# Kernel optimization log

Measured on AMD Instinct MI355X. Metric: run time of the kernel, lower is better.

Reference implementation:

```python
import jax, jax.numpy as jnp
import numpy as np

HID, NH, QLR, KVLR, QK, VH, RH = 7168, 128, 1536, 512, 128, 128, 64
EPS = 1.1920929e-07  # torch.finfo(float32).eps, RMSNorm eps=None default
ROPE_BASE = 10000.0


def _rmsnorm(x, w):
    return x * jax.lax.rsqrt(jnp.mean(x * x, axis=-1, keepdims=True) + EPS) * w


def _rope_tables(seq_len, dim):
    inv_freq = 1.0 / (ROPE_BASE ** (np.arange(0, dim, 2, dtype=np.float32) / dim))
    t = np.arange(seq_len, dtype=np.float32)
    freqs = np.outer(t, inv_freq)          # [S, dim/2]
    emb = np.concatenate([freqs, freqs], -1)  # [S, dim]
    return jnp.asarray(np.cos(emb)), jnp.asarray(np.sin(emb))


def _apply_rope(x, cos, sin):
    # x: [B, H, S, D]; rotate-half convention matching the torch module
    d = x.shape[-1]
    x1, x2 = x[..., : d // 2], x[..., d // 2 :]
    rotated = jnp.concatenate([-x2, x1], axis=-1)
    return x * cos + rotated * sin


def setup_inputs() -> dict:
    key = jax.random.key(0)
    ks = jax.random.split(key, 9)
    def w(k, out_dim, in_dim):
        return jax.random.normal(k, (out_dim, in_dim), jnp.float32) / np.sqrt(in_dim)
    return {
        "hidden_states": jax.random.normal(ks[0], (1, 1024, HID), jnp.float32),
        "w_q_down": w(ks[1], QLR, HID),
        "q_norm_w": jnp.ones((QLR,), jnp.float32),
        "w_q_up": w(ks[2], NH * (QK + RH), QLR),
        "w_kv_down": w(ks[3], KVLR + RH, HID),
        "kv_norm_w": jnp.ones((KVLR,), jnp.float32),
        "w_kv_up": w(ks[4], NH * (QK + VH), KVLR),
        "w_out": w(ks[5], HID, NH * VH),
    }


def reference(hidden_states, w_q_down, q_norm_w, w_q_up, w_kv_down, kv_norm_w, w_kv_up, w_out):
    B, S, _ = hidden_states.shape
    cos, sin = _rope_tables(S, RH)

    # Q path: down -> RMSNorm -> up, split into non-rope / rope parts
    c_q = jnp.einsum("bsh,qh->bsq", hidden_states, w_q_down)            # [B,S,QLR]
    q_cr = jnp.einsum("bsq,oq->bso", _rmsnorm(c_q, q_norm_w), w_q_up)   # [B,S,NH*(QK+RH)]
    q_cr = q_cr.reshape(B, S, NH, QK + RH).transpose(0, 2, 1, 3)        # [B,NH,S,QK+RH]
    q_c, q_r = q_cr[..., :QK], q_cr[..., QK:]

    # KV path: shared latent + MQA rope key
    ckv_kr = jnp.einsum("bsh,oh->bso", hidden_states, w_kv_down)        # [B,S,KVLR+RH]
    c_kv, k_r = ckv_kr[..., :KVLR], ckv_kr[..., KVLR:]
    k_r = k_r[:, None, :, :]                                            # [B,1,S,RH]
    kv = jnp.einsum("bsq,oq->bso", _rmsnorm(c_kv, kv_norm_w), w_kv_up)  # [B,S,NH*(QK+VH)]
    kv = kv.reshape(B, S, NH, QK + VH).transpose(0, 2, 1, 3)            # [B,NH,S,QK+VH]
    k_c, v = kv[..., :QK], kv[..., QK:]

    q_r = _apply_rope(q_r, cos, sin)
    k_r = _apply_rope(k_r, cos, sin)

    q = jnp.concatenate([q_c, q_r], axis=-1)                            # [B,NH,S,QK+RH]
    k = jnp.concatenate([k_c, jnp.broadcast_to(k_r, (B, NH, S, RH))], axis=-1)

    scale = 1.0 / np.sqrt(QK + RH)
    scores = jnp.einsum("bhqd,bhkd->bhqk", q, k) * scale
    attn = jax.nn.softmax(scores, axis=-1)
    o = jnp.einsum("bhqk,bhkd->bhqd", attn, v)                          # [B,NH,S,VH]
    o = o.transpose(0, 2, 1, 3).reshape(B, S, NH * VH)
    return jnp.einsum("bso,ho->bsh", o, w_out)
```

## Files before the change

kernel.cpp:

```cpp
#include <hip/hip_runtime.h>
#include <hip/hip_bf16.h>
#include <math.h>

#define HIDN 7168
#define NHEAD 128
#define QLRANK 1536
#define KVLRANK 512
#define QKD 128
#define VHD 128
#define RHD 64
#define SEQ 1024
#define RMS_EPS 1.1920929e-07f

typedef unsigned short u16;
typedef __attribute__((ext_vector_type(8))) short bf16x8;
typedef __attribute__((ext_vector_type(4))) float f32x4;
typedef __attribute__((ext_vector_type(8))) unsigned short u16x8;

__device__ __forceinline__ u16 f2bf(float f) {
    unsigned int u = __float_as_uint(f);
    unsigned int r = (u + 0x7FFFu + ((u >> 16) & 1u)) >> 16;
    return (u16)r;
}
__device__ __forceinline__ float bf2f(u16 v) {
    return __uint_as_float(((unsigned int)v) << 16);
}

__device__ __forceinline__ void gld_lds16(const u16* g, u16* l) {
    __builtin_amdgcn_global_load_lds(
        (const __attribute__((address_space(1))) unsigned int*)g,
        (__attribute__((address_space(3))) unsigned int*)l,
        16, 0, 0);
}

__global__ __launch_bounds__(256) void f32_to_bf16(const float* __restrict__ in,
                                                   u16* __restrict__ out, long n) {
    long i = ((long)blockIdx.x * blockDim.x + threadIdx.x) * 8;
    long stride = (long)gridDim.x * blockDim.x * 8;
    for (; i < n; i += stride) {
        float4 a = *(const float4*)(in + i);
        float4 b = *(const float4*)(in + i + 4);
        u16x8 o;
        o[0] = f2bf(a.x); o[1] = f2bf(a.y); o[2] = f2bf(a.z); o[3] = f2bf(a.w);
        o[4] = f2bf(b.x); o[5] = f2bf(b.y); o[6] = f2bf(b.z); o[7] = f2bf(b.w);
        *(u16x8*)(out + i) = o;
    }
}

template <int OUT_BF16>
__global__ __launch_bounds__(512) void gemm_bt(const u16* __restrict__ A,
                                               const u16* __restrict__ B,
                                               void* __restrict__ Cv,
                                               int M, int N, int Kslice, long ldk) {
    __shared__ u16 As[2 * 128 * 64];
    __shared__ u16 Bs[2 * 128 * 64];
    const int tid = threadIdx.x;
    const int lane = tid & 63;
    const int w = tid >> 6;
    const int wr = w >> 2, wc = w & 3;
    const int l15 = lane & 15, lg = lane >> 4;
    const int n0 = blockIdx.x * 128;
    const int m0 = blockIdx.y * 128;
    const long kbase = (long)blockIdx.z * Kslice;

    const u16* asrc[2];
    const u16* bsrc[2];
    int aoff[2];
#pragma unroll
    for (int i = 0; i < 2; ++i) {
        int r = (w * 2 + i) * 8 + (lane >> 3);
        int gc = (lane & 7) ^ (r & 7);
        asrc[i] = A + (long)(m0 + r) * ldk + kbase + gc * 8;
        int br = n0 + r; if (br >= N) br = N - 1;
        bsrc[i] = B + (long)br * ldk + kbase + gc * 8;
        aoff[i] = (w * 2 + i) * 512;
    }

    f32x4 acc[4][2];
    const f32x4 z = {0.f, 0.f, 0.f, 0.f};
#pragma unroll
    for (int i = 0; i < 4; ++i)
#pragma unroll
        for (int j = 0; j < 2; ++j) acc[i][j] = z;

    auto stage = [&](int bufi, int kofs) {
#pragma unroll
        for (int i = 0; i < 2; ++i) {
            gld_lds16(asrc[i] + kofs, As + bufi * 8192 + aoff[i]);
            gld_lds16(bsrc[i] + kofs, Bs + bufi * 8192 + aoff[i]);
        }
    };

    const int nsteps = Kslice >> 6;
    stage(0, 0);
    asm volatile("s_waitcnt vmcnt(0)" ::: "memory");
    __builtin_amdgcn_s_barrier();

    int cur = 0;
    for (int t = 0; t < nsteps; ++t) {
        if (t + 1 < nsteps) stage(cur ^ 1, (t + 1) * 64);
        const u16* Ab = As + cur * 8192;
        const u16* Bb = Bs + cur * 8192;
#pragma unroll
        for (int kk = 0; kk < 2; ++kk) {
            bf16x8 a[4], b[2];
#pragma unroll
            for (int i = 0; i < 4; ++i) {
                int row = wr * 64 + i * 16 + l15;
                a[i] = *(const bf16x8*)&Ab[row * 64 + ((kk * 4 + lg) ^ (row & 7)) * 8];
            }
#pragma unroll
            for (int j = 0; j < 2; ++j) {
                int row = wc * 32 + j * 16 + l15;
                b[j] = *(const bf16x8*)&Bb[row * 64 + ((kk * 4 + lg) ^ (row & 7)) * 8];
            }
#pragma unroll
            for (int i = 0; i < 4; ++i)
#pragma unroll
                for (int j = 0; j < 2; ++j)
                    acc[i][j] = __builtin_amdgcn_mfma_f32_16x16x32_bf16(a[i], b[j], acc[i][j], 0, 0, 0);
        }
        asm volatile("s_waitcnt vmcnt(0)" ::: "memory");
        __builtin_amdgcn_s_barrier();
        cur ^= 1;
    }

#pragma unroll
    for (int i = 0; i < 4; ++i)
#pragma unroll
        for (int j = 0; j < 2; ++j)
#pragma unroll
            for (int r = 0; r < 4; ++r) {
                int m = m0 + wr * 64 + i * 16 + lg * 4 + r;
                int n = n0 + wc * 32 + j * 16 + l15;
                if (n < N) {
                    if (OUT_BF16)
                        ((u16*)Cv)[(long)m * N + n] = f2bf(acc[i][j][r]);
                    else
                        ((float*)Cv)[(long)blockIdx.z * M * N + (long)m * N + n] = acc[i][j][r];
                }
            }
}

__global__ __launch_bounds__(256) void reduce_parts(const float* __restrict__ parts,
                                                    float* __restrict__ out,
                                                    int nparts, long mn) {
    long i = ((long)blockIdx.x * 256 + threadIdx.x) * 4;
    long stride = (long)gridDim.x * 256 * 4;
    for (; i < mn; i += stride) {
        float4 s = *(const float4*)(parts + i);
        for (int p = 1; p < nparts; ++p) {
            float4 v = *(const float4*)(parts + (long)p * mn + i);
            s.x += v.x; s.y += v.y; s.z += v.z; s.w += v.w;
        }
        *(float4*)(out + i) = s;
    }
}

__global__ __launch_bounds__(256) void rmsnorm_kernel(const float* __restrict__ x,
                                                      const float* __restrict__ w,
                                                      u16* __restrict__ y,
                                                      int stride, int norm_len) {
    const int row = blockIdx.x;
    const float* xr = x + (long)row * stride;
    float ss = 0.f;
    for (int i = threadIdx.x; i < norm_len; i += 256) {
        float v = xr[i];
        ss += v * v;
    }
#pragma unroll
    for (int off = 32; off > 0; off >>= 1) ss += __shfl_down(ss, off);
    __shared__ float partial[4];
    if ((threadIdx.x & 63) == 0) partial[threadIdx.x >> 6] = ss;
    __syncthreads();
    float tot = partial[0] + partial[1] + partial[2] + partial[3];
    float rs = 1.0f / sqrtf(tot / (float)norm_len + RMS_EPS);
    u16* yr = y + (long)row * norm_len;
    for (int i = threadIdx.x; i < norm_len; i += 256) yr[i] = f2bf(xr[i] * rs * w[i]);
}

__global__ void rope_tables(float* __restrict__ cos_t, float* __restrict__ sin_t) {
    int s = blockIdx.x;
    int i = threadIdx.x;
    float invf = powf(10000.0f, -((float)(2 * i) / 64.0f));
    float ang = (float)s * invf;
    cos_t[s * 32 + i] = cosf(ang);
    sin_t[s * 32 + i] = sinf(ang);
}

__global__ void rope_q(u16* __restrict__ q_cr, const float* __restrict__ cos_t,
                       const float* __restrict__ sin_t) {
    int s = blockIdx.x;
    int h = blockIdx.y * 2 + (threadIdx.x >> 5);
    int i = threadIdx.x & 31;
    u16* base = q_cr + (s * (NHEAD * 192) + h * 192 + QKD);
    float x1 = bf2f(base[i]);
    float x2 = bf2f(base[i + 32]);
    float c = cos_t[s * 32 + i], sn = sin_t[s * 32 + i];
    base[i]      = f2bf(x1 * c - x2 * sn);
    base[i + 32] = f2bf(x2 * c + x1 * sn);
}

__global__ void rope_k(const float* __restrict__ ckv_kr, const float* __restrict__ cos_t,
                       const float* __restrict__ sin_t, u16* __restrict__ kr) {
    int s = blockIdx.x;
    int i = threadIdx.x;
    if (i < 32) {
        const float* base = ckv_kr + (s * 576 + 512);
        float x1 = base[i], x2 = base[i + 32];
        float c = cos_t[s * 32 + i], sn = sin_t[s * 32 + i];
        kr[s * 64 + i]      = f2bf(x1 * c - x2 * sn);
        kr[s * 64 + i + 32] = f2bf(x2 * c + x1 * sn);
    }
}

__global__ __launch_bounds__(512) void mla_attn(const u16* __restrict__ q_cr,
                                                const u16* __restrict__ kv,
                                                const u16* __restrict__ kr,
                                                u16* __restrict__ o_g,
                                                const float* __restrict__ wsrc,
                                                u16* __restrict__ wdst,
                                                int do_conv) {
    __shared__ u16 ks[64][200];
    __shared__ u16 vts[128][72];
    __shared__ u16 p_lds[8][16][72];
    __shared__ u16 vtile[64][136];
    const int qb = blockIdx.x, h = blockIdx.y;
    const int s0q = qb * 128;
    const int tid = threadIdx.x, lane = tid & 63, w = tid >> 6;
    const int l15 = lane & 15, lg = lane >> 4;
    const float scale = 0.07216878364870323f;

    bf16x8 qreg[6];
    {
        const int qrow = s0q + w * 16 + l15;
#pragma unroll
        for (int kk = 0; kk < 6; ++kk)
            qreg[kk] = *(const bf16x8*)&q_cr[qrow * (NHEAD * 192) + h * 192 + kk * 32 + lg * 8];
    }

    const int krow0 = tid >> 4,           koff0 = (tid & 15) * 8;
    const int krow1 = (512 + tid) >> 4,   koff1 = ((512 + tid) & 15) * 8;
    const int rrow  = tid >> 3,           roff  = (tid & 7) * 8;
    const u16* kvp = kv + h * 256;
    const u16* kvv = kv + h * 256 + 128;

    u16x8 kreg0, kreg1, krreg, vreg0, vreg1;
    auto load_tile = [&](int s0k) {
        kreg0 = *(const u16x8*)&kvp[(long)(s0k + krow0) * 32768 + koff0];
        kreg1 = *(const u16x8*)&kvp[(long)(s0k + krow1) * 32768 + koff1];
        krreg = *(const u16x8*)&kr[(s0k + rrow) * 64 + roff];
        vreg0 = *(const u16x8*)&kvv[(long)(s0k + krow0) * 32768 + koff0];
        vreg1 = *(const u16x8*)&kvv[(long)(s0k + krow1) * 32768 + koff1];
    };

    const long cbase = ((long)(h * 8 + qb)) * 16 * 896;

    f32x4 o_acc[8];
    const f32x4 z = {0.f, 0.f, 0.f, 0.f};
#pragma unroll
    for (int d = 0; d < 8; ++d) o_acc[d] = z;
    float m_r[4], l_r[4];
#pragma unroll
    for (int r = 0; r < 4; ++r) { m_r[r] = -1e30f; l_r[r] = 0.f; }

    load_tile(0);

    for (int kt = 0; kt < 16; ++kt) {
        __syncthreads();
        *(u16x8*)&ks[krow0][koff0]      = kreg0;
        *(u16x8*)&ks[krow1][koff1]      = kreg1;
        *(u16x8*)&ks[rrow][128 + roff]  = krreg;
        *(u16x8*)&vtile[krow0][koff0]   = vreg0;
        *(u16x8*)&vtile[krow1][koff1]   = vreg1;
        __syncthreads();
        if (kt + 1 < 16) load_tile((kt + 1) * 64);

        if (do_conv) {
            long g0 = cbase + (long)kt * 896;
#pragma unroll
            for (int ci = 0; ci < 2; ++ci) {
                int gi = ci * 512 + tid;
                if (gi < 896) {
                    long g8 = (g0 + gi) * 8;
                    float4 a = *(const float4*)(wsrc + g8);
                    float4 b = *(const float4*)(wsrc + g8 + 4);
                    u16x8 o;
                    o[0] = f2bf(a.x); o[1] = f2bf(a.y); o[2] = f2bf(a.z); o[3] = f2bf(a.w);
                    o[4] = f2bf(b.x); o[5] = f2bf(b.y); o[6] = f2bf(b.z); o[7] = f2bf(b.w);
                    *(u16x8*)(wdst + g8) = o;
                }
            }
        }

        {
            const int dv = tid >> 2;
            const int sb = (tid & 3) << 4;
#pragma unroll
            for (int i = 0; i < 16; ++i)
                vts[dv][sb + i] = vtile[sb + i][dv];
        }

        f32x4 sf[4];
#pragma unroll
        for (int j = 0; j < 4; ++j) sf[j] = z;
        __builtin_amdgcn_s_setprio(1);
#pragma unroll
        for (int kk = 0; kk < 6; ++kk) {
            bf16x8 a = qreg[kk];
#pragma unroll
            for (int j = 0; j < 4; ++j) {
                bf16x8 b = *(const bf16x8*)&ks[j * 16 + l15][kk * 32 + lg * 8];
                sf[j] = __builtin_amdgcn_mfma_f32_16x16x32_bf16(a, b, sf[j], 0, 0, 0);
            }
        }
        __builtin_amdgcn_s_setprio(0);

        float p[4][4];
        float alpha[4];
#pragma unroll
        for (int r = 0; r < 4; ++r) {
            float mx = fmaxf(fmaxf(sf[0][r], sf[1][r]), fmaxf(sf[2][r], sf[3][r]));
#pragma unroll
            for (int off = 1; off < 16; off <<= 1) mx = fmaxf(mx, __shfl_xor(mx, off));
            mx *= scale;
            float mnew = fmaxf(m_r[r], mx);
            alpha[r] = __expf(m_r[r] - mnew);
            float rs = 0.f;
#pragma unroll
            for (int j = 0; j < 4; ++j) {
                float pv = __expf(sf[j][r] * scale - mnew);
                p[j][r] = pv;
                rs += pv;
            }
#pragma unroll
            for (int off = 1; off < 16; off <<= 1) rs += __shfl_xor(rs, off);
            l_r[r] = l_r[r] * alpha[r] + rs;
            m_r[r] = mnew;
        }
#pragma unroll
        for (int d = 0; d < 8; ++d)
#pragma unroll
            for (int r = 0; r < 4; ++r) o_acc[d][r] *= alpha[r];

#pragma unroll
        for (int j = 0; j < 4; ++j)
#pragma unroll
            for (int r = 0; r < 4; ++r)
                p_lds[w][lg * 4 + r][j * 16 + l15] = f2bf(p[j][r]);

        __syncthreads();

        __builtin_amdgcn_s_setprio(1);
#pragma unroll
        for (int kk2 = 0; kk2 < 2; ++kk2) {
            bf16x8 a = *(const bf16x8*)&p_lds[w][l15][kk2 * 32 + lg * 8];
#pragma unroll
            for (int d = 0; d < 8; ++d) {
                bf16x8 b = *(const bf16x8*)&vts[d * 16 + l15][kk2 * 32 + lg * 8];
                o_acc[d] = __builtin_amdgcn_mfma_f32_16x16x32_bf16(a, b, o_acc[d], 0, 0, 0);
            }
        }
        __builtin_amdgcn_s_setprio(0);
    }

#pragma unroll
    for (int d = 0; d < 8; ++d)
#pragma unroll
        for (int r = 0; r < 4; ++r) {
            int srow = s0q + w * 16 + lg * 4 + r;
            float v = o_acc[d][r] / l_r[r];
            o_g[srow * 16384 + h * 128 + d * 16 + l15] = f2bf(v);
        }
}

extern "C" void kernel_launch(void* const* d_in, const int* in_sizes, int n_in,
                              void* d_out, int out_size, void* d_ws, size_t ws_size,
                              hipStream_t stream) {
    const float* hs        = (const float*)d_in[0];
    const float* w_q_down  = (const float*)d_in[1];
    const float* q_norm_w  = (const float*)d_in[2];
    const float* w_q_up    = (const float*)d_in[3];
    const float* w_kv_down = (const float*)d_in[4];
    const float* kv_norm_w = (const float*)d_in[5];
    const float* w_kv_up   = (const float*)d_in[6];
    const float* w_out     = (const float*)d_in[7];
    float* out = (float*)d_out;
    char* ws = (char*)d_ws;

    const size_t SZ_KV   = (size_t)SEQ * 32768 * 2;
    const size_t SZ_QCR  = (size_t)SEQ * (NHEAD * 192) * 2;
    const size_t SZ_KR   = (size_t)SEQ * 64 * 2;
    const size_t SZ_OG   = (size_t)SEQ * 16384 * 2;
    const size_t SZ_TAB  = (size_t)SEQ * 32 * 4;
    const size_t SZ_WOUT = (size_t)HIDN * 16384 * 2;
    const size_t SZ_WB   = (size_t)24576 * 1536 * 2;
    const size_t SZ_PART = (size_t)4 * SEQ * QLRANK * 4;
    const size_t SZ_HS   = (size_t)SEQ * HIDN * 2;
    const size_t SZ_CQ   = (size_t)SEQ * QLRANK * 4;
    const size_t SZ_CQN  = (size_t)SEQ * QLRANK * 2;
    const size_t SZ_CKV  = (size_t)SEQ * 576 * 4;
    const size_t SZ_CKVN = (size_t)SEQ * KVLRANK * 2;

    size_t off = 0;
    u16* kvb     = (u16*)(ws + off); off += SZ_KV;
    u16* q_cr    = (u16*)(ws + off); off += SZ_QCR;
    u16* kr      = (u16*)(ws + off); off += SZ_KR;
    u16* o_g     = (u16*)(ws + off); off += SZ_OG;
    float* cos_t = (float*)(ws + off); off += SZ_TAB;
    float* sin_t = (float*)(ws + off); off += SZ_TAB;
    const size_t live_end = off;
    u16* wout_bf = (u16*)(ws + live_end);
    u16* W_BUF   = (u16*)(ws + live_end);
    float* parts = (float*)(ws + live_end + SZ_WB);
    size_t toff = live_end + SZ_WB + SZ_PART;
    u16* hs_bf    = (u16*)(ws + toff); toff += SZ_HS;
    float* c_q    = (float*)(ws + toff); toff += SZ_CQ;
    u16* cq_n     = (u16*)(ws + toff); toff += SZ_CQN;
    float* ckv_kr = (float*)(ws + toff); toff += SZ_CKV;
    u16* ckv_n    = (u16*)(ws + toff); toff += SZ_CKVN;
    const int fuse = (live_end + SZ_WOUT) <= ws_size;
    (void)in_sizes; (void)n_in; (void)out_size;

    rope_tables<<<dim3(SEQ), dim3(32), 0, stream>>>(cos_t, sin_t);
    f32_to_bf16<<<2048, 256, 0, stream>>>(hs, hs_bf, (long)SEQ * HIDN);

    f32_to_bf16<<<2048, 256, 0, stream>>>(w_q_down, W_BUF, (long)QLRANK * HIDN);
    gemm_bt<0><<<dim3(QLRANK / 128, SEQ / 128, 4), 512, 0, stream>>>(hs_bf, W_BUF, parts, SEQ, QLRANK, HIDN / 4, HIDN);
    reduce_parts<<<1024, 256, 0, stream>>>(parts, c_q, 4, (long)SEQ * QLRANK);
    rmsnorm_kernel<<<SEQ, 256, 0, stream>>>(c_q, q_norm_w, cq_n, QLRANK, QLRANK);

    f32_to_bf16<<<2048, 256, 0, stream>>>(w_q_up, W_BUF, (long)24576 * QLRANK);
    gemm_bt<1><<<dim3(24576 / 128, SEQ / 128), 512, 0, stream>>>(cq_n, W_BUF, q_cr, SEQ, 24576, QLRANK, QLRANK);

    f32_to_bf16<<<2048, 256, 0, stream>>>(w_kv_down, W_BUF, (long)576 * HIDN);
    gemm_bt<0><<<dim3(5, SEQ / 128, 8), 512, 0, stream>>>(hs_bf, W_BUF, parts, SEQ, 576, HIDN / 8, HIDN);
    reduce_parts<<<1024, 256, 0, stream>>>(parts, ckv_kr, 8, (long)SEQ * 576);
    rmsnorm_kernel<<<SEQ, 256, 0, stream>>>(ckv_kr, kv_norm_w, ckv_n, 576, KVLRANK);
    rope_k<<<SEQ, 64, 0, stream>>>(ckv_kr, cos_t, sin_t, kr);

    f32_to_bf16<<<2048, 256, 0, stream>>>(w_kv_up, W_BUF, (long)32768 * KVLRANK);
    gemm_bt<1><<<dim3(32768 / 128, SEQ / 128), 512, 0, stream>>>(ckv_n, W_BUF, kvb, SEQ, 32768, KVLRANK, KVLRANK);

    rope_q<<<dim3(SEQ, NHEAD / 2), 64, 0, stream>>>(q_cr, cos_t, sin_t);

    if (!fuse)
        f32_to_bf16<<<4096, 256, 0, stream>>>(w_out, wout_bf, (long)HIDN * 16384);
    mla_attn<<<dim3(SEQ / 128, NHEAD), 512, 0, stream>>>(q_cr, kvb, kr, o_g,
                                                         w_out, wout_bf, fuse ? 1 : 0);

    gemm_bt<0><<<dim3(HIDN / 128, SEQ / 128), 512, 0, stream>>>(o_g, wout_bf, out, SEQ, HIDN, 16384, 16384);
}
```

Measured before the change: 977.3 us.

## Pre-transpose V into a head-major layout and add an f32-weight output GEMM

Adds a build_vt kernel that writes V transposed per head, so the attention kernel loads V^T tiles directly into LDS. This removes the in-loop LDS transpose and one __syncthreads per tile. It also adds a GEMM that reads f32 w_out and converts it to bf16 on the fly, used when the workspace is too small to fuse the weight conversion, replacing the separate conversion pass. The cost is an extra V^T workspace buffer (which can push the fuse decision to the fallback path) plus an extra transpose kernel launch. Dropping the barrier before the P·V stage risks a race on p_lds unless the per-wave buffer makes it safe.

```diff
diff --git a/kernel.cpp b/kernel.cpp
--- a/kernel.cpp
+++ b/kernel.cpp
@@ -15,6 +15,7 @@
 typedef unsigned short u16;
 typedef __attribute__((ext_vector_type(8))) short bf16x8;
 typedef __attribute__((ext_vector_type(4))) float f32x4;
+typedef __attribute__((ext_vector_type(4))) unsigned short u16x4;
 typedef __attribute__((ext_vector_type(8))) unsigned short u16x8;
 
 __device__ __forceinline__ u16 f2bf(float f) {
@@ -142,6 +143,123 @@
             }
 }
 
+__global__ __launch_bounds__(512) void gemm_bt_f32b(const u16* __restrict__ A,
+                                                    const float* __restrict__ B,
+                                                    float* __restrict__ Cv,
+                                                    int M, int N, int K, long ldk) {
+    __shared__ u16 As[2 * 128 * 64];
+    __shared__ u16 Bs[2 * 128 * 64];
+    const int tid = threadIdx.x;
+    const int lane = tid & 63;
+    const int w = tid >> 6;
+    const int wr = w >> 2, wc = w & 3;
+    const int l15 = lane & 15, lg = lane >> 4;
+    const int n0 = blockIdx.x * 128;
+    const int m0 = blockIdx.y * 128;
+
+    const u16* asrc[2];
+    int aoff[2];
+#pragma unroll
+    for (int i = 0; i < 2; ++i) {
+        int r = (w * 2 + i) * 8 + (lane >> 3);
+        int gc = (lane & 7) ^ (r & 7);
+        asrc[i] = A + (long)(m0 + r) * ldk + gc * 8;
+        aoff[i] = (w * 2 + i) * 512;
+    }
+
+    const float* bsrcf[4];
+    int bdst[4];
+#pragma unroll
+    for (int i = 0; i < 4; ++i) {
+        int c = i * 64 + lane;
+        int rl = c >> 4, ch = c & 15;
+        int lrow = w * 16 + rl;
+        int gr = n0 + lrow; if (gr >= N) gr = N - 1;
+        bsrcf[i] = B + (long)gr * ldk + ch * 4;
+        bdst[i] = lrow * 64 + (((ch >> 1) ^ (lrow & 7)) * 8) + (ch & 1) * 4;
+    }
+
+    f32x4 acc[4][2];
+    const f32x4 z = {0.f, 0.f, 0.f, 0.f};
+#pragma unroll
+    for (int i = 0; i < 4; ++i)
+#pragma unroll
+        for (int j = 0; j < 2; ++j) acc[i][j] = z;
+
+    float4 bv[4];
+    auto stageA = [&](int bufi, int kofs) {
+#pragma unroll
+        for (int i = 0; i < 2; ++i)
+            gld_lds16(asrc[i] + kofs, As + bufi * 8192 + aoff[i]);
+    };
+    auto loadB = [&](int kofs) {
+#pragma unroll
+        for (int i = 0; i < 4; ++i) bv[i] = *(const float4*)(bsrcf[i] + kofs);
+    };
+    auto writeB = [&](int bufi) {
+#pragma unroll
+        for (int i = 0; i < 4; ++i) {
+            u16x4 o;
+            o[0] = f2bf(bv[i].x); o[1] = f2bf(bv[i].y);
+            o[2] = f2bf(bv[i].z); o[3] = f2bf(bv[i].w);
+            *(u16x4*)&Bs[bufi * 8192 + bdst[i]] = o;
+        }
+    };
+
+    const int nsteps = K >> 6;
+    stageA(0, 0);
+    loadB(0);
+    asm volatile("s_waitcnt vmcnt(0)" ::: "memory");
+    writeB(0);
+    asm volatile("s_waitcnt lgkmcnt(0)" ::: "memory");
+    __builtin_amdgcn_s_barrier();
+
+    int cur = 0;
+    for (int t = 0; t < nsteps; ++t) {
+        if (t + 1 < nsteps) {
+            stageA(cur ^ 1, (t + 1) * 64);
+            loadB((t + 1) * 64);
+        }
+        const u16* Ab = As + cur * 8192;
+        const u16* Bb = Bs + cur * 8192;
+#pragma unroll
+        for (int kk = 0; kk < 2; ++kk) {
+            bf16x8 a[4], b[2];
+#pragma unroll
+            for (int i = 0; i < 4; ++i) {
+                int row = wr * 64 + i * 16 + l15;
+                a[i] = *(const bf16x8*)&Ab[row * 64 + ((kk * 4 + lg) ^ (row & 7)) * 8];
+            }
+#pragma unroll
+            for (int j = 0; j < 2; ++j) {
+                int row = wc * 32 + j * 16 + l15;
+                b[j] = *(const bf16x8*)&Bb[row * 64 + ((kk * 4 + lg) ^ (row & 7)) * 8];
+            }
+#pragma unroll
+            for (int i = 0; i < 4; ++i)
+#pragma unroll
+                for (int j = 0; j < 2; ++j)
+                    acc[i][j] = __builtin_amdgcn_mfma_f32_16x16x32_bf16(a[i], b[j], acc[i][j], 0, 0, 0);
+        }
+        asm volatile("s_waitcnt vmcnt(0)" ::: "memory");
+        if (t + 1 < nsteps) writeB(cur ^ 1);
+        asm volatile("s_waitcnt lgkmcnt(0)" ::: "memory");
+        __builtin_amdgcn_s_barrier();
+        cur ^= 1;
+    }
+
+#pragma unroll
+    for (int i = 0; i < 4; ++i)
+#pragma unroll
+        for (int j = 0; j < 2; ++j)
+#pragma unroll
+            for (int r = 0; r < 4; ++r) {
+                int m = m0 + wr * 64 + i * 16 + lg * 4 + r;
+                int n = n0 + wc * 32 + j * 16 + l15;
+                if (n < N) Cv[(long)m * N + n] = acc[i][j][r];
+            }
+}
+
 __global__ __launch_bounds__(256) void reduce_parts(const float* __restrict__ parts,
                                                     float* __restrict__ out,
                                                     int nparts, long mn) {
@@ -214,9 +332,33 @@
     }
 }
 
+__global__ __launch_bounds__(256) void build_vt(const u16* __restrict__ kv,
+                                                u16* __restrict__ vT) {
+    __shared__ u16 vtile[64][136];
+    const int h = blockIdx.x, sb = blockIdx.y, s0 = sb * 64;
+    const int tid = threadIdx.x;
+#pragma unroll
+    for (int it = 0; it < 4; ++it) {
+        int c = it * 256 + tid;
+        int row = c >> 4;
+        int off8 = (c & 15) * 8;
+        *(u16x8*)&vtile[row][off8] =
+            *(const u16x8*)&kv[(s0 + row) * 32768 + h * 256 + 128 + off8];
+    }
+    __syncthreads();
+    const int sl = tid & 63;
+    const int dvb = tid >> 6;
+#pragma unroll
+    for (int it = 0; it < 32; ++it) {
+        int dv = dvb + it * 4;
+        vT[(h * 128 + dv) * 1024 + s0 + sl] = vtile[sl][dv];
+    }
+}
+
 __global__ __launch_bounds__(512) void mla_attn(const u16* __restrict__ q_cr,
                                                 const u16* __restrict__ kv,
                                                 const u16* __restrict__ kr,
+                                                const u16* __restrict__ vT,
                                                 u16* __restrict__ o_g,
                                                 const float* __restrict__ wsrc,
                                                 u16* __restrict__ wdst,
@@ -224,7 +366,6 @@
     __shared__ u16 ks[64][200];
     __shared__ u16 vts[128][72];
     __shared__ u16 p_lds[8][16][72];
-    __shared__ u16 vtile[64][136];
     const int qb = blockIdx.x, h = blockIdx.y;
     const int s0q = qb * 128;
     const int tid = threadIdx.x, lane = tid & 63, w = tid >> 6;
@@ -242,16 +383,18 @@
     const int krow0 = tid >> 4,           koff0 = (tid & 15) * 8;
     const int krow1 = (512 + tid) >> 4,   koff1 = ((512 + tid) & 15) * 8;
     const int rrow  = tid >> 3,           roff  = (tid & 7) * 8;
+    const int vdv0  = tid >> 3,           voff0 = (tid & 7) * 8;
+    const int vdv1  = (512 + tid) >> 3,   voff1 = ((512 + tid) & 7) * 8;
     const u16* kvp = kv + h * 256;
-    const u16* kvv = kv + h * 256 + 128;
+    const u16* vtp = vT + (long)(h * 128) * 1024;
 
     u16x8 kreg0, kreg1, krreg, vreg0, vreg1;
     auto load_tile = [&](int s0k) {
         kreg0 = *(const u16x8*)&kvp[(long)(s0k + krow0) * 32768 + koff0];
         kreg1 = *(const u16x8*)&kvp[(long)(s0k + krow1) * 32768 + koff1];
         krreg = *(const u16x8*)&kr[(s0k + rrow) * 64 + roff];
-        vreg0 = *(const u16x8*)&kvv[(long)(s0k + krow0) * 32768 + koff0];
-        vreg1 = *(const u16x8*)&kvv[(long)(s0k + krow1) * 32768 + koff1];
+        vreg0 = *(const u16x8*)&vtp[(long)vdv0 * 1024 + s0k + voff0];
+        vreg1 = *(const u16x8*)&vtp[(long)vdv1 * 1024 + s0k + voff1];
     };
 
     const long cbase = ((long)(h * 8 + qb)) * 16 * 896;
@@ -271,8 +414,8 @@
         *(u16x8*)&ks[krow0][koff0]      = kreg0;
         *(u16x8*)&ks[krow1][koff1]      = kreg1;
         *(u16x8*)&ks[rrow][128 + roff]  = krreg;
-        *(u16x8*)&vtile[krow0][koff0]   = vreg0;
-        *(u16x8*)&vtile[krow1][koff1]   = vreg1;
+        *(u16x8*)&vts[vdv0][voff0]      = vreg0;
+        *(u16x8*)&vts[vdv1][voff1]      = vreg1;
         __syncthreads();
         if (kt + 1 < 16) load_tile((kt + 1) * 64);
 
@@ -293,14 +436,6 @@
             }
         }
 
-        {
-            const int dv = tid >> 2;
-            const int sb = (tid & 3) << 4;
-#pragma unroll
-            for (int i = 0; i < 16; ++i)
-                vts[dv][sb + i] = vtile[sb + i][dv];
-        }
-
         f32x4 sf[4];
 #pragma unroll
         for (int j = 0; j < 4; ++j) sf[j] = z;
@@ -348,8 +483,6 @@
 #pragma unroll
             for (int r = 0; r < 4; ++r)
                 p_lds[w][lg * 4 + r][j * 16 + l15] = f2bf(p[j][r]);
-
-        __syncthreads();
 
         __builtin_amdgcn_s_setprio(1);
 #pragma unroll
@@ -391,8 +524,9 @@
     const size_t SZ_KV   = (size_t)SEQ * 32768 * 2;
     const size_t SZ_QCR  = (size_t)SEQ * (NHEAD * 192) * 2;
     const size_t SZ_KR   = (size_t)SEQ * 64 * 2;
+    const size_t SZ_TAB  = (size_t)SEQ * 32 * 4;
+    const size_t SZ_VT   = (size_t)NHEAD * 128 * 1024 * 2;
     const size_t SZ_OG   = (size_t)SEQ * 16384 * 2;
-    const size_t SZ_TAB  = (size_t)SEQ * 32 * 4;
     const size_t SZ_WOUT = (size_t)HIDN * 16384 * 2;
     const size_t SZ_WB   = (size_t)24576 * 1536 * 2;
     const size_t SZ_PART = (size_t)4 * SEQ * QLRANK * 4;
@@ -406,9 +540,10 @@
     u16* kvb     = (u16*)(ws + off); off += SZ_KV;
     u16* q_cr    = (u16*)(ws + off); off += SZ_QCR;
     u16* kr      = (u16*)(ws + off); off += SZ_KR;
-    u16* o_g     = (u16*)(ws + off); off += SZ_OG;
     float* cos_t = (float*)(ws + off); off += SZ_TAB;
     float* sin_t = (float*)(ws + off); off += SZ_TAB;
+    u16* vT      = (u16*)(ws + off); off += SZ_VT;
+    u16* o_g     = (u16*)(ws + off); off += SZ_OG;
     const size_t live_end = off;
     u16* wout_bf = (u16*)(ws + live_end);
     u16* W_BUF   = (u16*)(ws + live_end);
@@ -443,11 +578,14 @@
     gemm_bt<1><<<dim3(32768 / 128, SEQ / 128), 512, 0, stream>>>(ckv_n, W_BUF, kvb, SEQ, 32768, KVLRANK, KVLRANK);
 
     rope_q<<<dim3(SEQ, NHEAD / 2), 64, 0, stream>>>(q_cr, cos_t, sin_t);
-
-    if (!fuse)
-        f32_to_bf16<<<4096, 256, 0, stream>>>(w_out, wout_bf, (long)HIDN * 16384);
-    mla_attn<<<dim3(SEQ / 128, NHEAD), 512, 0, stream>>>(q_cr, kvb, kr, o_g,
+    build_vt<<<dim3(NHEAD, SEQ / 64), 256, 0, stream>>>(kvb, vT);
+
+    mla_attn<<<dim3(SEQ / 128, NHEAD), 512, 0, stream>>>(q_cr, kvb, kr, vT, o_g,
                                                          w_out, wout_bf, fuse ? 1 : 0);
 
-    gemm_bt<0><<<dim3(HIDN / 128, SEQ / 128), 512, 0, stream>>>(o_g, wout_bf, out, SEQ, HIDN, 16384, 16384);
-}
+    if (fuse) {
+        gemm_bt<0><<<dim3(HIDN / 128, SEQ / 128), 512, 0, stream>>>(o_g, wout_bf, out, SEQ, HIDN, 16384, 16384);
+    } else {
+        gemm_bt_f32b<<<dim3(HIDN / 128, SEQ / 128), 512, 0, stream>>>(o_g, w_out, out, SEQ, HIDN, 16384, 16384);
+    }
+}
```

After: 955.4 us. 1.02x faster.
